# Kernel tuning notes

Hardware: AMD Instinct MI355X
Metric: run time of the kernel (lower is better)

## Reference

```python
import jax, jax.numpy as jnp
import numpy as np

B, S, D, H, DFF = 2, 2048, 1024, 16, 4096
DK = D // H
EPS = float(np.finfo(np.float32).eps)  # torch RMSNorm default eps = finfo eps


def rmsnorm(x, g):
    var = jnp.mean(x * x, axis=-1, keepdims=True)
    return x * jax.lax.rsqrt(var + EPS) * g


def rope_cos_sin(seq_len, dim, base=10000.0):
    inv_freq = 1.0 / (base ** (jnp.arange(0, dim, 2, dtype=jnp.float32) / dim))
    t = jnp.arange(seq_len, dtype=jnp.float32)
    freqs = jnp.outer(t, inv_freq)            # [S, dim/2]
    emb = jnp.concatenate([freqs, freqs], -1)  # [S, dim]
    return jnp.cos(emb), jnp.sin(emb)


def rotate_half(x):
    x1, x2 = x[..., : x.shape[-1] // 2], x[..., x.shape[-1] // 2:]
    return jnp.concatenate([-x2, x1], axis=-1)


def setup_inputs() -> dict:
    key = jax.random.key(0)
    ks = jax.random.split(key, 16)
    sc = 0.02
    return {
        "x": jax.random.normal(ks[0], (B, S, D), jnp.float32),
        "wq": jax.random.normal(ks[1], (D, D), jnp.float32) * sc,
        "bq": jnp.zeros((D,), jnp.float32),
        "wk": jax.random.normal(ks[2], (D, D), jnp.float32) * sc,
        "bk": jnp.zeros((D,), jnp.float32),
        "wv": jax.random.normal(ks[3], (D, D), jnp.float32) * sc,
        "bv": jnp.zeros((D,), jnp.float32),
        "wo": jax.random.normal(ks[4], (D, D), jnp.float32) * sc,
        "bo": jnp.zeros((D,), jnp.float32),
        "w1": jax.random.normal(ks[5], (D, DFF), jnp.float32) * sc,
        "b1": jnp.zeros((DFF,), jnp.float32),
        "w2": jax.random.normal(ks[6], (DFF, D), jnp.float32) * sc,
        "b2": jnp.zeros((D,), jnp.float32),
        "g1": jnp.ones((D,), jnp.float32),
        "g2": jnp.ones((D,), jnp.float32),
    }


def reference(x, wq, bq, wk, bk, wv, bv, wo, bo, w1, b1, w2, b2, g1, g2):
    b, s, d = x.shape
    # --- self-attention sublayer (pre-RMSNorm residual) ---
    h = rmsnorm(x, g1)
    q = (h @ wq + bq).reshape(b, s, H, DK).transpose(0, 2, 1, 3)  # [B,H,S,dk]
    k = (h @ wk + bk).reshape(b, s, H, DK).transpose(0, 2, 1, 3)
    v = (h @ wv + bv).reshape(b, s, H, DK).transpose(0, 2, 1, 3)
    cos, sin = rope_cos_sin(s, DK)
    cos = cos[None, None]  # [1,1,S,dk]
    sin = sin[None, None]
    q = q * cos + rotate_half(q) * sin
    k = k * cos + rotate_half(k) * sin
    scores = jnp.einsum("bhqd,bhkd->bhqk", q, k) / jnp.sqrt(jnp.float32(DK))
    p = jax.nn.softmax(scores, axis=-1)
    o = jnp.einsum("bhqk,bhkd->bhqd", p, v)
    o = o.transpose(0, 2, 1, 3).reshape(b, s, d)
    attn_out = o @ wo + bo
    x = x + attn_out
    # --- feed-forward sublayer ---
    h2 = rmsnorm(x, g2)
    ff = jax.nn.relu(h2 @ w1 + b1) @ w2 + b2
    return x + ff
```

## Files before the change

### kernel.cpp

```cpp
#include <hip/hip_runtime.h>
#include <math.h>

typedef unsigned short u16;
typedef __attribute__((ext_vector_type(8))) short bf16x8;
typedef __attribute__((ext_vector_type(4))) float f32x4;
typedef __attribute__((ext_vector_type(4))) unsigned int u32x4;

#define B_ 2
#define S_ 2048
#define D_ 1024
#define H_ 16
#define DK_ 64
#define DFF_ 4096
#define EPS_ 1.1920928955078125e-07f
#define EXP2SC 0.18033688011112042f

__device__ __forceinline__ float bf2f(u16 u) {
  unsigned int v = ((unsigned int)u) << 16;
  return __builtin_bit_cast(float, v);
}
__device__ __forceinline__ u16 f2bf(float f) {
  unsigned int x = __builtin_bit_cast(unsigned int, f);
  x += 0x7fffu + ((x >> 16) & 1u);
  return (u16)(x >> 16);
}

typedef __attribute__((address_space(3))) unsigned int lds_uint;
typedef const __attribute__((address_space(1))) unsigned int glb_uint;
__device__ __forceinline__ void gload16(const void* g, void* l) {
  __builtin_amdgcn_global_load_lds((glb_uint*)g, (lds_uint*)l, 16, 0, 0);
}

__device__ __forceinline__ unsigned int cvtpk(float lo, float hi) {
  unsigned int d;
  asm("v_cvt_pk_bf16_f32 %0, %1, %2" : "=v"(d) : "v"(lo), "v"(hi));
  return d;
}
__device__ __forceinline__ void plswap32(unsigned int& a, unsigned int& b) {
  asm("v_permlane32_swap_b32 %0, %1" : "+v"(a), "+v"(b));
}
__device__ __forceinline__ void plswap16(unsigned int& a, unsigned int& b) {
  asm("v_permlane16_swap_b32 %0, %1" : "+v"(a), "+v"(b));
}

__device__ __forceinline__ void xcd_swizzle(int& bx, int& by) {
  const int nx = gridDim.x;
  const int nwg = nx * gridDim.y;
  const int lin = blockIdx.y * nx + blockIdx.x;
  const int swz = (lin & 7) * (nwg >> 3) + (lin >> 3);
  bx = swz % nx;
  by = swz / nx;
}

__global__ __launch_bounds__(256) void prep_qkvo(
    const float* __restrict__ wq, const float* __restrict__ wk,
    const float* __restrict__ wv, const float* __restrict__ wo,
    u16* __restrict__ qkvT, u16* __restrict__ woT,
    float* __restrict__ cosT, float* __restrict__ sinT) {
  __shared__ float t[32][33];
  const int bid = blockIdx.x;
  const int tid = threadIdx.x;
  if (bid < 4096) {
    const int m = bid >> 10;
    const int tb = bid & 1023;
    const float* src = (m == 0) ? wq : (m == 1) ? wk : (m == 2) ? wv : wo;
    u16* dst = (m == 3) ? woT : qkvT + (size_t)m * D_ * D_;
    const int c0 = (tb & 31) * 32, r0 = (tb >> 5) * 32;
    const int tx = tid & 31, ty = tid >> 5;
#pragma unroll
    for (int i = 0; i < 32; i += 8)
      t[ty + i][tx] = src[(size_t)(r0 + ty + i) * D_ + (c0 + tx)];
    __syncthreads();
#pragma unroll
    for (int i = 0; i < 32; i += 8)
      dst[(size_t)(c0 + ty + i) * D_ + (r0 + tx)] = f2bf(t[tx][ty + i]);
  } else {
    const int idx = (bid - 4096) * 256 + tid;
    const int s = idx >> 5, i = idx & 31;
    double inv = exp(((double)(-2 * i) / (double)DK_) * log(10000.0));
    double ang = (double)s * inv;
    cosT[idx] = (float)cos(ang);
    sinT[idx] = (float)sin(ang);
  }
}

__global__ __launch_bounds__(256) void prep_w12(
    const float* __restrict__ w1, const float* __restrict__ w2,
    u16* __restrict__ w1T, u16* __restrict__ w2T) {
  __shared__ float t[32][33];
  const int bid = blockIdx.x;
  const int tid = threadIdx.x;
  const int tx = tid & 31, ty = tid >> 5;
  if (bid < 4096) {
    const int c0 = (bid & 127) * 32, r0 = (bid >> 7) * 32;
#pragma unroll
    for (int i = 0; i < 32; i += 8)
      t[ty + i][tx] = w1[(size_t)(r0 + ty + i) * DFF_ + (c0 + tx)];
    __syncthreads();
#pragma unroll
    for (int i = 0; i < 32; i += 8)
      w1T[(size_t)(c0 + ty + i) * D_ + (r0 + tx)] = f2bf(t[tx][ty + i]);
  } else {
    const int b2 = bid - 4096;
    const int c0 = (b2 & 31) * 32, r0 = (b2 >> 5) * 32;
#pragma unroll
    for (int i = 0; i < 32; i += 8)
      t[ty + i][tx] = w2[(size_t)(r0 + ty + i) * D_ + (c0 + tx)];
    __syncthreads();
#pragma unroll
    for (int i = 0; i < 32; i += 8)
      w2T[(size_t)(c0 + ty + i) * DFF_ + (r0 + tx)] = f2bf(t[tx][ty + i]);
  }
}

__global__ __launch_bounds__(256) void rmsnorm_k(const float* __restrict__ X,
                                                 const float* __restrict__ g,
                                                 u16* __restrict__ out) {
  const int row = blockIdx.x;
  const float* xr = X + (size_t)row * D_;
  u16* orow = out + (size_t)row * D_;
  const int tid = threadIdx.x;
  float vals[4];
  float s = 0.f;
#pragma unroll
  for (int j = 0; j < 4; j++) {
    float v = xr[tid + j * 256];
    vals[j] = v;
    s += v * v;
  }
#pragma unroll
  for (int off = 32; off > 0; off >>= 1) s += __shfl_down(s, off, 64);
  __shared__ float red[4];
  __shared__ float ssc;
  int lane = tid & 63, wave = tid >> 6;
  if (lane == 0) red[wave] = s;
  __syncthreads();
  if (tid == 0) ssc = 1.0f / sqrtf((red[0] + red[1] + red[2] + red[3]) * (1.0f / D_) + EPS_);
  __syncthreads();
  float sc = ssc;
#pragma unroll
  for (int j = 0; j < 4; j++) {
    int i = tid + j * 256;
    orow[i] = f2bf(vals[j] * sc * g[i]);
  }
}

#define GEMM_KLOOP(APTR, BPTR, KLEN, KLD)                                              \
  for (int k0 = 0; k0 < (KLEN); k0 += 64) {                                            \
    _Pragma("unroll")                                                                  \
    for (int p = 0; p < 2; p++) {                                                      \
      _Pragma("unroll")                                                                \
      for (int c = wave; c < BM / 16; c += 4) {                                        \
        const u16* gp = (APTR) + (size_t)(m0 + c * 16 + lrow) * (KLD) + k0 + p * 32 + lcol; \
        gload16(gp, (char*)As + __builtin_amdgcn_readfirstlane(p * (BM * 64) + c * 1024)); \
      }                                                                                \
      _Pragma("unroll")                                                                \
      for (int c = wave; c < BN / 16; c += 4) {                                        \
        const u16* gp = (BPTR) + (size_t)(n0 + c * 16 + lrow) * (KLD) + k0 + p * 32 + lcol; \
        gload16(gp, (char*)Bs + __builtin_amdgcn_readfirstlane(p * (BN * 64) + c * 1024)); \
      }                                                                                \
    }                                                                                  \
    __syncthreads();                                                                   \
    _Pragma("unroll")                                                                  \
    for (int p = 0; p < 2; p++) {                                                      \
      bf16x8 af[WR], bfv[WC];                                                          \
      _Pragma("unroll")                                                                \
      for (int i = 0; i < WR; i++)                                                     \
        af[i] = *(const bf16x8*)&As[p * (BM * 32) + (wm + i * 16 + l16) * 32 + quad * 8]; \
      _Pragma("unroll")                                                                \
      for (int j = 0; j < WC; j++)                                                     \
        bfv[j] = *(const bf16x8*)&Bs[p * (BN * 32) + (wn + j * 16 + l16) * 32 + quad * 8]; \
      _Pragma("unroll")                                                                \
      for (int i = 0; i < WR; i++)                                                     \
        _Pragma("unroll")                                                              \
        for (int j = 0; j < WC; j++)                                                   \
          acc[i][j] = __builtin_amdgcn_mfma_f32_16x16x32_bf16(af[i], bfv[j], acc[i][j], 0, 0, 0); \
    }                                                                                  \
    __syncthreads();                                                                   \
  }

template <int MODE, int WR, int WC>
__global__ __launch_bounds__(256) void gemm_bt(
    const u16* __restrict__ A, const u16* __restrict__ Bt, const float* __restrict__ bias,
    u16* __restrict__ outB, float* __restrict__ outF, const float* __restrict__ resF,
    int M, int N, int K) {
  constexpr int BM = 2 * WR * 16;
  constexpr int BN = 2 * WC * 16;
  __shared__ u16 As[BM * 64];
  __shared__ u16 Bs[BN * 64];
  const int tid = threadIdx.x;
  const int wave = tid >> 6, lane = tid & 63, quad = lane >> 4, l16 = lane & 15;
  const int wm = (wave >> 1) * (WR * 16), wn = (wave & 1) * (WC * 16);
  int bx, by;
  xcd_swizzle(bx, by);
  const int m0 = by * BM, n0 = bx * BN;
  const int lrow = lane >> 2, lcol = (lane & 3) * 8;
  f32x4 acc[WR][WC] = {};
  GEMM_KLOOP(A, Bt, K, K)
#pragma unroll
  for (int i = 0; i < WR; i++)
#pragma unroll
    for (int j = 0; j < WC; j++) {
      int col = n0 + wn + j * 16 + l16;
      float bv = bias[col];
#pragma unroll
      for (int r = 0; r < 4; r++) {
        int row = m0 + wm + i * 16 + quad * 4 + r;
        size_t off = (size_t)row * N + col;
        float v = acc[i][j][r] + bv;
        if constexpr (MODE == 1) v = fmaxf(v, 0.f);
        if constexpr (MODE == 2) outF[off] = v + resF[off];
        else outB[off] = f2bf(v);
      }
    }
}

__global__ __launch_bounds__(256) void gemm_qkv(
    const u16* __restrict__ A, const u16* __restrict__ Bt,
    const float* __restrict__ bq, const float* __restrict__ bk, const float* __restrict__ bv,
    const float* __restrict__ cosT, const float* __restrict__ sinT,
    u16* __restrict__ Qb, u16* __restrict__ Kb, u16* __restrict__ VT, int M, int K) {
  constexpr int WR = 4, WC = 4;
  constexpr int BM = 128, BN = 128;
  __shared__ u16 As[BM * 64];
  __shared__ u16 Bs[BN * 64];
  const int tid = threadIdx.x;
  const int wave = tid >> 6, lane = tid & 63, quad = lane >> 4, l16 = lane & 15;
  const int wm = (wave >> 1) * 64, wn = (wave & 1) * 64;
  int bx, by;
  xcd_swizzle(bx, by);
  const int m0 = by * BM, n0 = bx * BN;
  const int lrow = lane >> 2, lcol = (lane & 3) * 8;
  f32x4 acc[WR][WC] = {};
  GEMM_KLOOP(A, Bt, K, K)
  const int g = n0 >> 10;
  if (g < 2) {
    u16* dst = (g == 0) ? Qb : Kb;
    const float* bias = (g == 0) ? bq : bk;
    const float scq = (g == 0) ? EXP2SC : 1.0f;
#pragma unroll
    for (int i = 0; i < WR; i++)
#pragma unroll
      for (int jp = 0; jp < 2; jp++) {
        int col0 = n0 + wn + jp * 16 + l16;
        int c0 = col0 & 1023;
        float bv0 = bias[c0], bv1 = bias[c0 + 32];
        int irot = jp * 16 + l16;
        int row0 = m0 + wm + i * 16 + quad * 4;
#pragma unroll
        for (int r = 0; r < 4; r++) {
          int row = row0 + r;
          int s2 = row & 2047;
          float cs = cosT[s2 * 32 + irot];
          float sn = sinT[s2 * 32 + irot];
          float x0 = acc[i][jp][r] + bv0;
          float x1 = acc[i][jp + 2][r] + bv1;
          dst[(size_t)row * D_ + c0]      = f2bf((x0 * cs - x1 * sn) * scq);
          dst[(size_t)row * D_ + c0 + 32] = f2bf((x1 * cs + x0 * sn) * scq);
        }
      }
  } else {
#pragma unroll
    for (int i = 0; i < WR; i++)
#pragma unroll
      for (int j = 0; j < WC; j++) {
        int col = n0 + wn + j * 16 + l16;
        int c = col & 1023;
        float bvv = bv[c];
        int row0 = m0 + wm + i * 16 + quad * 4;
        int hh = c >> 6, dk = c & 63;
        int b = row0 >> 11, s2 = row0 & 2047;
        ushort4 pv;
        pv.x = f2bf(acc[i][j][0] + bvv);
        pv.y = f2bf(acc[i][j][1] + bvv);
        pv.z = f2bf(acc[i][j][2] + bvv);
        pv.w = f2bf(acc[i][j][3] + bvv);
        *(ushort4*)&VT[(((size_t)(b * H_ + hh)) * DK_ + dk) * S_ + s2] = pv;
      }
  }
}

template <int WR, int WC>
__global__ __launch_bounds__(256) void gemm_splitk(
    const u16* __restrict__ A, const u16* __restrict__ Bt, const float* __restrict__ bias,
    float* outF, int M, int N, int Kslice, int Kld) {
  constexpr int BM = 2 * WR * 16;
  constexpr int BN = 2 * WC * 16;
  __shared__ u16 As[BM * 64];
  __shared__ u16 Bs[BN * 64];
  const int tid = threadIdx.x;
  const int wave = tid >> 6, lane = tid & 63, quad = lane >> 4, l16 = lane & 15;
  const int wm = (wave >> 1) * (WR * 16), wn = (wave & 1) * (WC * 16);
  int bx, by;
  xcd_swizzle(bx, by);
  const int m0 = by * BM, n0 = bx * BN;
  const int lrow = lane >> 2, lcol = (lane & 3) * 8;
  const u16* Ao = A + (size_t)blockIdx.z * Kslice;
  const u16* Bo = Bt + (size_t)blockIdx.z * Kslice;
  f32x4 acc[WR][WC] = {};
  GEMM_KLOOP(Ao, Bo, Kslice, Kld)
  const bool addb = (blockIdx.z == 0);
#pragma unroll
  for (int i = 0; i < WR; i++)
#pragma unroll
    for (int j = 0; j < WC; j++) {
      int col = n0 + wn + j * 16 + l16;
      float bv = addb ? bias[col] : 0.f;
#pragma unroll
      for (int r = 0; r < 4; r++) {
        int row = m0 + wm + i * 16 + quad * 4 + r;
        unsafeAtomicAdd(&outF[(size_t)row * N + col], acc[i][j][r] + bv);
      }
    }
}

__device__ __forceinline__ void softmax_pack(f32x4 s0, f32x4 s1, f32x4 s2, f32x4 s3,
                                             bf16x8& pf0, bf16x8& pf1) {
  f32x4 p0, p1, p2, p3;
#pragma unroll
  for (int r = 0; r < 4; r++) {
    p0[r] = exp2f(s0[r]);
    p1[r] = exp2f(s1[r]);
    p2[r] = exp2f(s2[r]);
    p3[r] = exp2f(s3[r]);
  }
  unsigned int X0 = cvtpk(p0[0], p0[1]), X1 = cvtpk(p0[2], p0[3]);
  unsigned int Y0 = cvtpk(p1[0], p1[1]), Y1 = cvtpk(p1[2], p1[3]);
  unsigned int Z0 = cvtpk(p2[0], p2[1]), Z1 = cvtpk(p2[2], p2[3]);
  unsigned int W0 = cvtpk(p3[0], p3[1]), W1 = cvtpk(p3[2], p3[3]);
  plswap32(X0, Y0); plswap16(X0, Y0);
  plswap32(X1, Y1); plswap16(X1, Y1);
  plswap32(Z0, W0); plswap16(Z0, W0);
  plswap32(Z1, W1); plswap16(Z1, W1);
  u32x4 lo = {X0, X1, Y0, Y1};
  u32x4 hi = {Z0, Z1, W0, W1};
  pf0 = __builtin_bit_cast(bf16x8, lo);
  pf1 = __builtin_bit_cast(bf16x8, hi);
}

__global__ __launch_bounds__(256, 2) void flash_attn(u16* __restrict__ Q,
                                                     const u16* __restrict__ Kg,
                                                     const u16* __restrict__ VT) {
  const int bh = blockIdx.y;
  const int b = bh >> 4, h = bh & 15;
  const int q0 = blockIdx.x * 128;
  const int tid = threadIdx.x;
  const int wave = tid >> 6, lane = tid & 63, quad = lane >> 4, l16 = lane & 15;
  const size_t base = (size_t)b * S_ * D_ + h * DK_;
  const size_t vbase = (size_t)bh * DK_ * S_;

  __shared__ u16 Ks[2][8192];
  __shared__ u16 Vts[2][8192];

  const int kkey = wave * 32 + (lane >> 3);
  const int kcol = ((lane & 7) ^ (lane >> 3)) * 8;
  const u16* kp0 = Kg + base + (size_t)kkey * D_ + kcol;
  const int vdk0 = wave * 16 + (lane >> 4);
  const int vsel = lane & 15;
  const u16* vp0 = VT + vbase + (size_t)vdk0 * S_;

#define STAGE(BU, KT)                                                                  \
  _Pragma("unroll")                                                                    \
  for (int c = 0; c < 4; c++) {                                                        \
    gload16(kp0 + (size_t)((KT) + c * 8) * D_,                                         \
            (char*)Ks + __builtin_amdgcn_readfirstlane((BU) * 16384 + wave * 4096 + c * 1024)); \
    int vdk = vdk0 + c * 4;                                                            \
    gload16(vp0 + (size_t)(c * 4) * S_ + (KT) + ((vsel ^ (vdk & 7)) * 8),              \
            (char*)Vts + __builtin_amdgcn_readfirstlane((BU) * 16384 + wave * 4096 + c * 1024)); \
  }

  STAGE(0, 0)

  const size_t qoffA = base + (size_t)(q0 + wave * 32 + l16) * D_ + quad * 8;
  const size_t qoffB = qoffA + (size_t)16 * D_;
  bf16x8 qa0 = *(const bf16x8*)(Q + qoffA);
  bf16x8 qa1 = *(const bf16x8*)(Q + qoffA + 32);
  bf16x8 qb0 = *(const bf16x8*)(Q + qoffB);
  bf16x8 qb1 = *(const bf16x8*)(Q + qoffB + 32);

  f32x4 oa[4] = {}, ob[4] = {};
  f32x4 lsa_acc = {}, lsb_acc = {};
  const u32x4 onesu = {0x3F803F80u, 0x3F803F80u, 0x3F803F80u, 0x3F803F80u};
  const bf16x8 ones = __builtin_bit_cast(bf16x8, onesu);
  const int sw = (l16 & 7) << 4;

#define TILE(BU)                                                                       \
  {                                                                                    \
    const char* KsB = (const char*)Ks + (BU) * 16384;                                  \
    const char* VtsB = (const char*)Vts + (BU) * 16384;                                \
    f32x4 sa[2][4] = {}, sb[2][4] = {};                                                \
    __builtin_amdgcn_s_setprio(1);                                                     \
    _Pragma("unroll")                                                                  \
    for (int half = 0; half < 2; half++) {                                             \
      _Pragma("unroll")                                                                \
      for (int nt = 0; nt < 4; nt++) {                                                 \
        const int kr = half * 64 + nt * 16 + l16;                                      \
        const char* krow = KsB + kr * 128;                                             \
        bf16x8 k0 = *(const bf16x8*)(krow + ((quad * 16) ^ sw));                       \
        bf16x8 k1 = *(const bf16x8*)(krow + ((64 + quad * 16) ^ sw));                  \
        sa[half][nt] = __builtin_amdgcn_mfma_f32_16x16x32_bf16(k0, qa0, sa[half][nt], 0, 0, 0); \
        sa[half][nt] = __builtin_amdgcn_mfma_f32_16x16x32_bf16(k1, qa1, sa[half][nt], 0, 0, 0); \
        sb[half][nt] = __builtin_amdgcn_mfma_f32_16x16x32_bf16(k0, qb0, sb[half][nt], 0, 0, 0); \
        sb[half][nt] = __builtin_amdgcn_mfma_f32_16x16x32_bf16(k1, qb1, sb[half][nt], 0, 0, 0); \
      }                                                                                \
    }                                                                                  \
    __builtin_amdgcn_s_setprio(0);                                                     \
    bf16x8 pa[2][2], pb[2][2];                                                         \
    _Pragma("unroll")                                                                  \
    for (int half = 0; half < 2; half++) {                                             \
      softmax_pack(sa[half][0], sa[half][1], sa[half][2], sa[half][3], pa[half][0], pa[half][1]); \
      softmax_pack(sb[half][0], sb[half][1], sb[half][2], sb[half][3], pb[half][0], pb[half][1]); \
    }                                                                                  \
    __builtin_amdgcn_s_setprio(1);                                                     \
    _Pragma("unroll")                                                                  \
    for (int half = 0; half < 2; half++) {                                             \
      lsa_acc = __builtin_amdgcn_mfma_f32_16x16x32_bf16(pa[half][0], ones, lsa_acc, 0, 0, 0); \
      lsa_acc = __builtin_amdgcn_mfma_f32_16x16x32_bf16(pa[half][1], ones, lsa_acc, 0, 0, 0); \
      lsb_acc = __builtin_amdgcn_mfma_f32_16x16x32_bf16(pb[half][0], ones, lsb_acc, 0, 0, 0); \
      lsb_acc = __builtin_amdgcn_mfma_f32_16x16x32_bf16(pb[half][1], ones, lsb_acc, 0, 0, 0); \
      _Pragma("unroll")                                                                \
      for (int nt = 0; nt < 4; nt++) {                                                 \
        const int vr = nt * 16 + l16;                                                  \
        const char* vrow = VtsB + vr * 256;                                            \
        bf16x8 v0 = *(const bf16x8*)(vrow + ((half * 128 + quad * 16) ^ sw));          \
        bf16x8 v1 = *(const bf16x8*)(vrow + ((half * 128 + 64 + quad * 16) ^ sw));     \
        oa[nt] = __builtin_amdgcn_mfma_f32_16x16x32_bf16(pa[half][0], v0, oa[nt], 0, 0, 0); \
        oa[nt] = __builtin_amdgcn_mfma_f32_16x16x32_bf16(pa[half][1], v1, oa[nt], 0, 0, 0); \
        ob[nt] = __builtin_amdgcn_mfma_f32_16x16x32_bf16(pb[half][0], v0, ob[nt], 0, 0, 0); \
        ob[nt] = __builtin_amdgcn_mfma_f32_16x16x32_bf16(pb[half][1], v1, ob[nt], 0, 0, 0); \
      }                                                                                \
    }                                                                                  \
    __builtin_amdgcn_s_setprio(0);                                                     \
  }

  for (int kt = 0; kt < S_; kt += 256) {
    __syncthreads();
    STAGE(1, kt + 128)
    TILE(0)
    __syncthreads();
    if (kt + 256 < S_) { STAGE(0, kt + 256) }
    TILE(1)
  }
#undef STAGE
#undef TILE

#pragma unroll
  for (int r = 0; r < 4; r++) {
    float inva = 1.0f / lsa_acc[r];
    float invb = 1.0f / lsb_acc[r];
    const size_t aoff = base + (size_t)(q0 + wave * 32 + quad * 4 + r) * D_;
    const size_t boff = aoff + (size_t)16 * D_;
#pragma unroll
    for (int nt = 0; nt < 4; nt++) {
      Q[aoff + nt * 16 + l16] = f2bf(oa[nt][r] * inva);
      Q[boff + nt * 16 + l16] = f2bf(ob[nt][r] * invb);
    }
  }
}

extern "C" void kernel_launch(void* const* d_in, const int* in_sizes, int n_in,
                              void* d_out, int out_size, void* d_ws, size_t ws_size,
                              hipStream_t stream) {
  const float* x  = (const float*)d_in[0];
  const float* wq = (const float*)d_in[1];
  const float* bq = (const float*)d_in[2];
  const float* wk = (const float*)d_in[3];
  const float* bk = (const float*)d_in[4];
  const float* wv = (const float*)d_in[5];
  const float* bv = (const float*)d_in[6];
  const float* wo = (const float*)d_in[7];
  const float* bo = (const float*)d_in[8];
  const float* w1 = (const float*)d_in[9];
  const float* b1 = (const float*)d_in[10];
  const float* w2 = (const float*)d_in[11];
  const float* b2 = (const float*)d_in[12];
  const float* g1 = (const float*)d_in[13];
  const float* g2 = (const float*)d_in[14];

  char* ws = (char*)d_ws;
  const size_t MB = 1024 * 1024;
  u16* qkvT = (u16*)(ws + 0 * MB);
  u16* woT  = (u16*)(ws + 6 * MB);
  u16* h    = (u16*)(ws + 8 * MB);
  u16* Qb   = (u16*)(ws + 16 * MB);
  u16* Kb   = (u16*)(ws + 24 * MB);
  float* cosT = (float*)(ws + 32 * MB);
  float* sinT = (float*)(ws + 32 * MB + 256 * 1024);
  u16* w2T  = (u16*)(ws + 0 * MB);
  u16* w1T  = (u16*)(ws + 16 * MB);
  u16* f1   = (u16*)(ws + 24 * MB);
  u16* h2   = h;
  u16* Ob   = Qb;
  u16* VT   = (u16*)d_out;
  float* x2 = (float*)d_out;
  const bool bigffn = (ws_size >= 57 * MB);

  const int MS = B_ * S_;
  prep_qkvo<<<4096 + S_ * 32 / 256, 256, 0, stream>>>(wq, wk, wv, wo, qkvT, woT, cosT, sinT);
  rmsnorm_k<<<MS, 256, 0, stream>>>(x, g1, h);
  gemm_qkv<<<dim3(3 * D_ / 128, MS / 128), 256, 0, stream>>>(h, qkvT, bq, bk, bv, cosT, sinT, Qb, Kb, VT, MS, D_);
  flash_attn<<<dim3(S_ / 128, B_ * H_), 256, 0, stream>>>(Qb, Kb, VT);
  gemm_bt<2, 4, 2><<<dim3(D_ / 64, MS / 128), 256, 0, stream>>>(Ob, woT, bo, nullptr, x2, x, MS, D_, D_);

  prep_w12<<<8192, 256, 0, stream>>>(w1, w2, w1T, w2T);
  rmsnorm_k<<<MS, 256, 0, stream>>>(x2, g2, h2);
  if (bigffn) {
    gemm_bt<1, 4, 4><<<dim3(DFF_ / 128, MS / 128), 256, 0, stream>>>(h2, w1T, b1, f1, nullptr, nullptr, MS, DFF_, D_);
    gemm_splitk<4, 4><<<dim3(D_ / 128, MS / 128, 2), 256, 0, stream>>>(f1, w2T, b2, x2, MS, D_, 2048, DFF_);
  } else {
    for (int i = 0; i < 2; i++) {
      const u16* h2h = h2 + (size_t)i * 2048 * D_;
      float* x2h = x2 + (size_t)i * 2048 * D_;
      gemm_bt<1, 4, 4><<<dim3(DFF_ / 128, 2048 / 128), 256, 0, stream>>>(h2h, w1T, b1, f1, nullptr, nullptr, 2048, DFF_, D_);
      gemm_splitk<4, 4><<<dim3(D_ / 128, 2048 / 128, 2), 256, 0, stream>>>(f1, w2T, b2, x2h, 2048, D_, 2048, DFF_);
    }
  }
  (void)in_sizes; (void)n_in; (void)out_size;
}
```

Measured before the change: 373.9 us.

## Double-buffer GEMM K-loop halves to overlap global loads with MFMA compute

The shared GEMM K-loop macro now treats the two 32-wide halves of each 64-wide K tile as ping-pong LDS buffers. It loads the next half while the MFMAs consume the current one, instead of loading a full tile, syncing, computing and syncing again. This is meant to hide global-to-LDS latency behind matrix math, at the cost of an extra barrier per half and a tighter dependency on correct wait ordering. Separately, the non-bigffn FFN down-projection path raises split-K from 2 to 4 slices of 1024 to add parallelism.

```diff
diff --git a/kernel.cpp b/kernel.cpp
--- a/kernel.cpp
+++ b/kernel.cpp
@@ -145,38 +145,48 @@
   }
 }
 
-#define GEMM_KLOOP(APTR, BPTR, KLEN, KLD)                                              \
-  for (int k0 = 0; k0 < (KLEN); k0 += 64) {                                            \
+#define GK_STAGE(BU, K0)                                                               \
+  _Pragma("unroll")                                                                    \
+  for (int c = wave; c < BM / 16; c += 4) {                                            \
+    const u16* gp = gkA + (size_t)(m0 + c * 16 + lrow) * gkLD + (K0) + lcol;           \
+    gload16(gp, (char*)As + __builtin_amdgcn_readfirstlane((BU) * (BM * 64) + c * 1024)); \
+  }                                                                                    \
+  _Pragma("unroll")                                                                    \
+  for (int c = wave; c < BN / 16; c += 4) {                                            \
+    const u16* gp = gkB + (size_t)(n0 + c * 16 + lrow) * gkLD + (K0) + lcol;           \
+    gload16(gp, (char*)Bs + __builtin_amdgcn_readfirstlane((BU) * (BN * 64) + c * 1024)); \
+  }
+
+#define GK_COMPUTE(BU)                                                                 \
+  {                                                                                    \
+    bf16x8 af[WR], bfv[WC];                                                            \
     _Pragma("unroll")                                                                  \
-    for (int p = 0; p < 2; p++) {                                                      \
-      _Pragma("unroll")                                                                \
-      for (int c = wave; c < BM / 16; c += 4) {                                        \
-        const u16* gp = (APTR) + (size_t)(m0 + c * 16 + lrow) * (KLD) + k0 + p * 32 + lcol; \
-        gload16(gp, (char*)As + __builtin_amdgcn_readfirstlane(p * (BM * 64) + c * 1024)); \
-      }                                                                                \
-      _Pragma("unroll")                                                                \
-      for (int c = wave; c < BN / 16; c += 4) {                                        \
-        const u16* gp = (BPTR) + (size_t)(n0 + c * 16 + lrow) * (KLD) + k0 + p * 32 + lcol; \
-        gload16(gp, (char*)Bs + __builtin_amdgcn_readfirstlane(p * (BN * 64) + c * 1024)); \
-      }                                                                                \
-    }                                                                                  \
-    __syncthreads();                                                                   \
+    for (int i = 0; i < WR; i++)                                                       \
+      af[i] = *(const bf16x8*)&As[(BU) * (BM * 32) + (wm + i * 16 + l16) * 32 + quad * 8]; \
     _Pragma("unroll")                                                                  \
-    for (int p = 0; p < 2; p++) {                                                      \
-      bf16x8 af[WR], bfv[WC];                                                          \
-      _Pragma("unroll")                                                                \
-      for (int i = 0; i < WR; i++)                                                     \
-        af[i] = *(const bf16x8*)&As[p * (BM * 32) + (wm + i * 16 + l16) * 32 + quad * 8]; \
+    for (int j = 0; j < WC; j++)                                                       \
+      bfv[j] = *(const bf16x8*)&Bs[(BU) * (BN * 32) + (wn + j * 16 + l16) * 32 + quad * 8]; \
+    _Pragma("unroll")                                                                  \
+    for (int i = 0; i < WR; i++)                                                       \
       _Pragma("unroll")                                                                \
       for (int j = 0; j < WC; j++)                                                     \
-        bfv[j] = *(const bf16x8*)&Bs[p * (BN * 32) + (wn + j * 16 + l16) * 32 + quad * 8]; \
-      _Pragma("unroll")                                                                \
-      for (int i = 0; i < WR; i++)                                                     \
-        _Pragma("unroll")                                                              \
-        for (int j = 0; j < WC; j++)                                                   \
-          acc[i][j] = __builtin_amdgcn_mfma_f32_16x16x32_bf16(af[i], bfv[j], acc[i][j], 0, 0, 0); \
+        acc[i][j] = __builtin_amdgcn_mfma_f32_16x16x32_bf16(af[i], bfv[j], acc[i][j], 0, 0, 0); \
+  }
+
+#define GEMM_KLOOP(APTR, BPTR, KLEN, KLD)                                              \
+  {                                                                                    \
+    const u16* gkA = (APTR);                                                           \
+    const u16* gkB = (BPTR);                                                           \
+    const int gkLD = (KLD);                                                            \
+    GK_STAGE(0, 0)                                                                     \
+    for (int k0 = 0; k0 < (KLEN); k0 += 64) {                                          \
+      __syncthreads();               \
+      GK_STAGE(1, k0 + 32)                       \
+      GK_COMPUTE(0)                                                                    \
+      __syncthreads();                    \
+      if (k0 + 64 < (KLEN)) { GK_STAGE(0, k0 + 64) }                                   \
+      GK_COMPUTE(1)                                                                    \
     }                                                                                  \
-    __syncthreads();                                                                   \
   }
 
 template <int MODE, int WR, int WC>
@@ -512,7 +522,7 @@
       const u16* h2h = h2 + (size_t)i * 2048 * D_;
       float* x2h = x2 + (size_t)i * 2048 * D_;
       gemm_bt<1, 4, 4><<<dim3(DFF_ / 128, 2048 / 128), 256, 0, stream>>>(h2h, w1T, b1, f1, nullptr, nullptr, 2048, DFF_, D_);
-      gemm_splitk<4, 4><<<dim3(D_ / 128, 2048 / 128, 2), 256, 0, stream>>>(f1, w2T, b2, x2h, 2048, D_, 2048, DFF_);
+      gemm_splitk<4, 4><<<dim3(D_ / 128, 2048 / 128, 4), 256, 0, stream>>>(f1, w2T, b2, x2h, 2048, D_, 1024, DFF_);
     }
   }
   (void)in_sizes; (void)n_in; (void)out_size;
```

Result: slower. 385.8 us (+3.2%).
